# Performance work log

Hardware: AMD Instinct MI355X
Metric: run time of the kernel (lower is better)

The kernel has to match this reference:

```python
import jax, jax.numpy as jnp
import numpy as np

B, T, EI, EO = 64, 512, 1024, 1024

def setup_inputs() -> dict:
    key = jax.random.key(0)
    k1, k2, k3, k4 = jax.random.split(key, 4)
    x = jax.random.normal(k1, (B, T, EI), dtype=jnp.float32)
    h0 = jax.random.normal(k2, (B, EO), dtype=jnp.float32)
    # match nn.Linear init scale roughly (uniform +-1/sqrt(fan_in))
    wxh = jax.random.uniform(k3, (EI, EO), dtype=jnp.float32, minval=-1.0, maxval=1.0) / np.sqrt(EI)
    whf = jax.random.uniform(k4, (EO, EO), dtype=jnp.float32, minval=-1.0, maxval=1.0) / np.sqrt(EO)
    return {"x": x, "h0": h0, "wxh": wxh, "whf": whf}

def reference(x, h0, wxh, whf):
    # Minimal GRU (all NOT_MUTATED flags = 1.0):
    #   ft = sigmoid(h_{t-1} @ whf); gt = tanh(x_t @ wxh)
    #   h_t = (1 - ft) * h_{t-1} + ft * gt; out_t = h_t
    def step(h, xt):
        ft = jax.nn.sigmoid(h @ whf)          # [B, EO]
        gt = jnp.tanh(xt @ wxh)               # [B, EO]
        h = (1.0 - ft) * h + ft * gt
        return h, h
    xT = jnp.swapaxes(x, 0, 1)                # [T, B, EI]
    hT, outs = jax.lax.scan(step, h0, xT)     # outs: [T, B, EO]
    outs = jnp.swapaxes(outs, 0, 1)           # [B, T, EO]
    return outs, hT
```

## Files before the change

kernel.cpp:

```cpp
#include <hip/hip_runtime.h>
#include <stdint.h>

#define B_   64
#define T_   512
#define EI_  1024
#define EO_  1024

typedef __attribute__((ext_vector_type(4))) float  f32x4;
typedef __attribute__((ext_vector_type(8))) short  s16x8;
typedef __attribute__((ext_vector_type(4))) unsigned short u16x4;

__device__ __forceinline__ unsigned short f2bf(float f) {
    union { float f; unsigned int u; } v; v.f = f;
    unsigned int r = v.u + 0x7FFFu + ((v.u >> 16) & 1u);
    return (unsigned short)(r >> 16);
}

__global__ void prep_kernel(const float* __restrict__ wxh, const float* __restrict__ whf,
                            const float* __restrict__ h0,
                            unsigned short* __restrict__ wxhT, unsigned short* __restrict__ whfT,
                            unsigned short* __restrict__ hbf1, unsigned int* __restrict__ flags)
{
    __shared__ unsigned short Ts[64][72];
    const int bid = blockIdx.x;
    const float* src = (bid & 1) ? whf : wxh;
    unsigned short* dst = (bid & 1) ? whfT : wxhT;
    const int tile = bid >> 1;
    const int k0 = (tile >> 4) * 64, n0 = (tile & 15) * 64;
    const int tid = threadIdx.x;

    #pragma unroll
    for (int it = 0; it < 4; ++it) {
        int r  = it * 16 + (tid >> 4);
        int cq = tid & 15;
        f32x4 v = *(const f32x4*)(src + (size_t)(k0 + r) * EO_ + n0 + cq * 4);
        #pragma unroll
        for (int i = 0; i < 4; ++i) Ts[cq * 4 + i][r] = f2bf(v[i]);
    }
    __syncthreads();
    #pragma unroll
    for (int it = 0; it < 2; ++it) {
        int n = it * 32 + (tid >> 3);
        int c = tid & 7;
        s16x8 v = *(const s16x8*)(&Ts[n][c * 8]);
        *(s16x8*)(dst + (size_t)(n0 + n) * EI_ + k0 + c * 8) = v;
    }
    if (bid < 256) {
        int j = bid * 256 + tid;
        hbf1[j] = f2bf(h0[j]);
    }
    if (bid == 0 && tid < 64) flags[tid] = 0u;
}

__launch_bounds__(256, 2)
__global__ void gemm_g_kernel(const float* __restrict__ X,
                              const unsigned short* __restrict__ WT,
                              float* __restrict__ out)
{
    __shared__ alignas(16) unsigned short As[128 * 72];
    __shared__ alignas(16) unsigned short Bs[128 * 72];

    const int bid = blockIdx.x;
    const int bn = bid & 7, bm = bid >> 3;
    const int m0 = bm * 128, n0 = bn * 128;
    const int tid  = threadIdx.x;
    const int lane = tid & 63, w = tid >> 6;
    const int wr = w >> 1, wc = w & 1;
    const int l15 = lane & 15, lg = lane >> 4;

    f32x4 acc[4][4] = {};

    for (int kt = 0; kt < EI_ / 64; ++kt) {
        const int k0 = kt * 64;
        #pragma unroll
        for (int p = 0; p < 8; ++p) {
            int row = p * 16 + (tid >> 4);
            int kq  = tid & 15;
            f32x4 v = *(const f32x4*)(X + (size_t)(m0 + row) * EI_ + k0 + kq * 4);
            u16x4 hv;
            hv[0] = f2bf(v[0]); hv[1] = f2bf(v[1]); hv[2] = f2bf(v[2]); hv[3] = f2bf(v[3]);
            *(u16x4*)(&As[row * 72 + kq * 4]) = hv;
        }
        #pragma unroll
        for (int p = 0; p < 4; ++p) {
            int n  = p * 32 + (tid >> 3);
            int kq = tid & 7;
            s16x8 v = *(const s16x8*)(WT + (size_t)(n0 + n) * EI_ + k0 + kq * 8);
            *(s16x8*)(&Bs[n * 72 + kq * 8]) = v;
        }
        __syncthreads();
        #pragma unroll
        for (int kk = 0; kk < 2; ++kk) {
            s16x8 a[4], b[4];
            #pragma unroll
            for (int mt = 0; mt < 4; ++mt)
                a[mt] = *(const s16x8*)(&As[(wr * 64 + mt * 16 + l15) * 72 + kk * 32 + lg * 8]);
            #pragma unroll
            for (int nt = 0; nt < 4; ++nt)
                b[nt] = *(const s16x8*)(&Bs[(wc * 64 + nt * 16 + l15) * 72 + kk * 32 + lg * 8]);
            #pragma unroll
            for (int mt = 0; mt < 4; ++mt)
                #pragma unroll
                for (int nt = 0; nt < 4; ++nt)
                    acc[mt][nt] = __builtin_amdgcn_mfma_f32_16x16x32_bf16(a[mt], b[nt], acc[mt][nt], 0, 0, 0);
        }
        __syncthreads();
    }
    #pragma unroll
    for (int mt = 0; mt < 4; ++mt) {
        #pragma unroll
        for (int nt = 0; nt < 4; ++nt) {
            #pragma unroll
            for (int r = 0; r < 4; ++r) {
                int row = wr * 64 + mt * 16 + lg * 4 + r;
                int col = wc * 64 + nt * 16 + l15;
                float s = acc[mt][nt][r];
                float e = __expf(2.f * s);
                out[(size_t)(m0 + row) * EO_ + n0 + col] = 1.f - 2.f / (e + 1.f);
            }
        }
    }
}

__launch_bounds__(1024, 1)
__global__ void recur_kernel(const float* __restrict__ h0,
                             const unsigned short* __restrict__ whfT,
                             unsigned short* hbf,
                             unsigned int* flags,
                             float* out)
{
    __shared__ alignas(16) unsigned short Ws[64 * 1024];
    __shared__ float Sred[4 * 16 * 68];

    const int bid = blockIdx.x;
    const int cb = bid >> 4;
    const int cc = bid & 15;
    const int tid = threadIdx.x;
    const int lane = tid & 63, w = tid >> 6;
    const int l15 = lane & 15, lg = lane >> 4;
    const int nq = w & 3, kq = w >> 2;

    {
        int c  = tid >> 4;
        int k8 = tid & 15;
        #pragma unroll
        for (int p = 0; p < 8; ++p) {
            int k = (k8 + p * 16) * 8;
            s16x8 v = *(const s16x8*)(whfT + (size_t)(cc * 64 + c) * EO_ + k);
            *(s16x8*)(&Ws[c * 1024 + (k ^ ((c & 7) << 3))]) = v;
        }
    }

    const int row = tid >> 6;
    const int col = tid & 63;
    const int b = cb * 16 + row;
    const int j = cc * 64 + col;
    float h = h0[(size_t)b * EO_ + j];

    const unsigned int* flg = flags + cb * 16;
    const int wc_frag = nq * 16 + l15;
    const int ksw = (wc_frag & 7) << 3;

    __syncthreads();

    for (int t = 0; t < T_; ++t) {
        size_t oidx = ((size_t)b * T_ + t) * EO_ + j;
        float g = out[oidx];

        if (t > 0 && w == 0) {
            unsigned int want = (unsigned int)t;
            int spins = 0;
            for (;;) {
                unsigned int f = (lane < 16)
                    ? __hip_atomic_load(&flg[lane], __ATOMIC_RELAXED, __HIP_MEMORY_SCOPE_AGENT)
                    : want;
                if (__ballot(f >= want) == ~0ULL) break;
                if (++spins > (1 << 20)) break;
            }
        }
        __syncthreads();

        const unsigned short* arow = hbf + (size_t)((t & 1) ^ 1) * (B_ * EO_)
                                   + (size_t)(cb * 16 + l15) * EO_;
        unsigned long long a0[8], a1[8];
        #pragma unroll
        for (int kk = 0; kk < 8; ++kk) {
            int k = kq * 256 + kk * 32 + lg * 8;
            a0[kk] = __hip_atomic_load((const unsigned long long*)(arow + k),
                                       __ATOMIC_RELAXED, __HIP_MEMORY_SCOPE_AGENT);
            a1[kk] = __hip_atomic_load((const unsigned long long*)(arow + k + 4),
                                       __ATOMIC_RELAXED, __HIP_MEMORY_SCOPE_AGENT);
        }
        f32x4 acc = {0.f, 0.f, 0.f, 0.f};
        #pragma unroll
        for (int kk = 0; kk < 8; ++kk) {
            int k = kq * 256 + kk * 32 + lg * 8;
            s16x8 bb = *(const s16x8*)(&Ws[wc_frag * 1024 + (k ^ ksw)]);
            union { unsigned long long u[2]; s16x8 v; } av;
            av.u[0] = a0[kk]; av.u[1] = a1[kk];
            acc = __builtin_amdgcn_mfma_f32_16x16x32_bf16(av.v, bb, acc, 0, 0, 0);
        }
        #pragma unroll
        for (int r = 0; r < 4; ++r)
            Sred[kq * (16 * 68) + (lg * 4 + r) * 68 + nq * 16 + l15] = acc[r];
        __syncthreads();

        float s = Sred[row * 68 + col]        + Sred[1088 + row * 68 + col]
                + Sred[2176 + row * 68 + col] + Sred[3264 + row * 68 + col];
        float fg = 1.f / (1.f + __expf(-s));
        h = (1.f - fg) * h + fg * g;
        out[oidx] = h;

        unsigned short mybf = f2bf(h);
        unsigned int other = (unsigned int)__shfl_xor((int)(unsigned int)mybf, 1);
        if (!(lane & 1)) {
            unsigned int packed = (unsigned int)mybf | (other << 16);
            __hip_atomic_store((unsigned int*)(hbf + (size_t)(t & 1) * (B_ * EO_)
                                               + (size_t)b * EO_ + j),
                               packed, __ATOMIC_RELAXED, __HIP_MEMORY_SCOPE_AGENT);
        }
        __syncthreads();
        if (tid == 0)
            __hip_atomic_store(&flags[cb * 16 + cc], (unsigned int)(t + 1),
                               __ATOMIC_RELAXED, __HIP_MEMORY_SCOPE_AGENT);
    }
    out[(size_t)B_ * T_ * EO_ + (size_t)b * EO_ + j] = h;
}

extern "C" void kernel_launch(void* const* d_in, const int* in_sizes, int n_in,
                              void* d_out, int out_size, void* d_ws, size_t ws_size,
                              hipStream_t stream)
{
    const float* x   = (const float*)d_in[0];
    const float* h0  = (const float*)d_in[1];
    const float* wxh = (const float*)d_in[2];
    const float* whf = (const float*)d_in[3];
    float* out = (float*)d_out;

    char* ws = (char*)d_ws;
    unsigned short* whfT  = (unsigned short*)(ws);
    unsigned short* wxhT  = (unsigned short*)(ws + (size_t)2 * 1024 * 1024);
    unsigned short* hbf   = (unsigned short*)(ws + (size_t)4 * 1024 * 1024);
    unsigned int*   flags = (unsigned int*)  (ws + (size_t)4 * 1024 * 1024 + 512 * 1024);

    prep_kernel<<<512, 256, 0, stream>>>(wxh, whf, h0, wxhT, whfT, hbf + B_ * EO_, flags);
    gemm_g_kernel<<<2048, 256, 0, stream>>>(x, wxhT, out);
    recur_kernel<<<64, 1024, 0, stream>>>(h0, whfT, hbf, flags, out);
}
```

Measured before the change: 4.495 ms.

## Hold recurrent weights in registers and sync per-wave instead of per-block

The recurrent kernel now runs 256-thread blocks in which each wave keeps its 16-column slice of the recurrent weight matrix in registers (32 fragments) and computes the full K=1024 reduction itself. This removes the LDS weight tile, the cross-wave LDS reduction and all __syncthreads in the time loop. Each wave publishes its own progress flag, and consumers spin on 64 per-wave flags. The cost is heavy register pressure (Wf plus a 64-entry A buffer), which risks spills, along with more flag polling traffic and four times more serial MFMAs per wave on the critical path.

New measurement: 5.628 ms. 25.2% more time.

```diff
diff --git a/kernel.cpp b/kernel.cpp
--- a/kernel.cpp
+++ b/kernel.cpp
@@ -49,7 +49,7 @@
         int j = bid * 256 + tid;
         hbf1[j] = f2bf(h0[j]);
     }
-    if (bid == 0 && tid < 64) flags[tid] = 0u;
+    if (bid == 0) flags[tid] = 0u;
 }
 
 __launch_bounds__(256, 2)
@@ -122,109 +122,98 @@
     }
 }
 
-__launch_bounds__(1024, 1)
+__launch_bounds__(256, 1)
 __global__ void recur_kernel(const float* __restrict__ h0,
                              const unsigned short* __restrict__ whfT,
                              unsigned short* hbf,
                              unsigned int* flags,
                              float* out)
 {
-    __shared__ alignas(16) unsigned short Ws[64 * 1024];
-    __shared__ float Sred[4 * 16 * 68];
-
     const int bid = blockIdx.x;
-    const int cb = bid >> 4;
-    const int cc = bid & 15;
+    const int g = bid >> 4;
+    const int q = bid & 15;
     const int tid = threadIdx.x;
     const int lane = tid & 63, w = tid >> 6;
     const int l15 = lane & 15, lg = lane >> 4;
-    const int nq = w & 3, kq = w >> 2;
-
-    {
-        int c  = tid >> 4;
-        int k8 = tid & 15;
-        #pragma unroll
-        for (int p = 0; p < 8; ++p) {
-            int k = (k8 + p * 16) * 8;
-            s16x8 v = *(const s16x8*)(whfT + (size_t)(cc * 64 + c) * EO_ + k);
-            *(s16x8*)(&Ws[c * 1024 + (k ^ ((c & 7) << 3))]) = v;
-        }
-    }
-
-    const int row = tid >> 6;
-    const int col = tid & 63;
-    const int b = cb * 16 + row;
-    const int j = cc * 64 + col;
-    float h = h0[(size_t)b * EO_ + j];
-
-    const unsigned int* flg = flags + cb * 16;
-    const int wc_frag = nq * 16 + l15;
-    const int ksw = (wc_frag & 7) << 3;
-
-    __syncthreads();
+    const int wid = q * 4 + w;
+    const int col = wid * 16 + l15;
+    const int rowbase = g * 16 + lg * 4;
+
+    s16x8 Wf[32];
+    #pragma unroll
+    for (int kk = 0; kk < 32; ++kk)
+        Wf[kk] = *(const s16x8*)(whfT + (size_t)col * EO_ + kk * 32 + lg * 8);
+
+    float h[4];
+    #pragma unroll
+    for (int r = 0; r < 4; ++r)
+        h[r] = h0[(size_t)(rowbase + r) * EO_ + col];
+
+    unsigned int* const flg = flags + g * 64;
 
     for (int t = 0; t < T_; ++t) {
-        size_t oidx = ((size_t)b * T_ + t) * EO_ + j;
-        float g = out[oidx];
-
-        if (t > 0 && w == 0) {
-            unsigned int want = (unsigned int)t;
+        float gv[4];
+        #pragma unroll
+        for (int r = 0; r < 4; ++r)
+            gv[r] = out[((size_t)(rowbase + r) * T_ + t) * EO_ + col];
+
+        if (t > 0) {
+            const unsigned int want = (unsigned int)t;
             int spins = 0;
             for (;;) {
-                unsigned int f = (lane < 16)
-                    ? __hip_atomic_load(&flg[lane], __ATOMIC_RELAXED, __HIP_MEMORY_SCOPE_AGENT)
-                    : want;
+                unsigned int f = __hip_atomic_load(&flg[lane], __ATOMIC_RELAXED,
+                                                   __HIP_MEMORY_SCOPE_AGENT);
                 if (__ballot(f >= want) == ~0ULL) break;
                 if (++spins > (1 << 20)) break;
             }
         }
-        __syncthreads();
+        asm volatile("" ::: "memory");
 
         const unsigned short* arow = hbf + (size_t)((t & 1) ^ 1) * (B_ * EO_)
-                                   + (size_t)(cb * 16 + l15) * EO_;
-        unsigned long long a0[8], a1[8];
-        #pragma unroll
-        for (int kk = 0; kk < 8; ++kk) {
-            int k = kq * 256 + kk * 32 + lg * 8;
-            a0[kk] = __hip_atomic_load((const unsigned long long*)(arow + k),
-                                       __ATOMIC_RELAXED, __HIP_MEMORY_SCOPE_AGENT);
-            a1[kk] = __hip_atomic_load((const unsigned long long*)(arow + k + 4),
-                                       __ATOMIC_RELAXED, __HIP_MEMORY_SCOPE_AGENT);
-        }
-        f32x4 acc = {0.f, 0.f, 0.f, 0.f};
-        #pragma unroll
-        for (int kk = 0; kk < 8; ++kk) {
-            int k = kq * 256 + kk * 32 + lg * 8;
-            s16x8 bb = *(const s16x8*)(&Ws[wc_frag * 1024 + (k ^ ksw)]);
+                                   + (size_t)(g * 16 + l15) * EO_ + lg * 8;
+        unsigned long long abuf[64];
+        #pragma unroll
+        for (int kk = 0; kk < 32; ++kk) {
+            abuf[2 * kk]     = __hip_atomic_load((const unsigned long long*)(arow + kk * 32),
+                                                 __ATOMIC_RELAXED, __HIP_MEMORY_SCOPE_AGENT);
+            abuf[2 * kk + 1] = __hip_atomic_load((const unsigned long long*)(arow + kk * 32 + 4),
+                                                 __ATOMIC_RELAXED, __HIP_MEMORY_SCOPE_AGENT);
+        }
+        f32x4 acc[4] = {};
+        #pragma unroll
+        for (int kk = 0; kk < 32; ++kk) {
             union { unsigned long long u[2]; s16x8 v; } av;
-            av.u[0] = a0[kk]; av.u[1] = a1[kk];
-            acc = __builtin_amdgcn_mfma_f32_16x16x32_bf16(av.v, bb, acc, 0, 0, 0);
-        }
-        #pragma unroll
-        for (int r = 0; r < 4; ++r)
-            Sred[kq * (16 * 68) + (lg * 4 + r) * 68 + nq * 16 + l15] = acc[r];
-        __syncthreads();
-
-        float s = Sred[row * 68 + col]        + Sred[1088 + row * 68 + col]
-                + Sred[2176 + row * 68 + col] + Sred[3264 + row * 68 + col];
-        float fg = 1.f / (1.f + __expf(-s));
-        h = (1.f - fg) * h + fg * g;
-        out[oidx] = h;
-
-        unsigned short mybf = f2bf(h);
-        unsigned int other = (unsigned int)__shfl_xor((int)(unsigned int)mybf, 1);
-        if (!(lane & 1)) {
-            unsigned int packed = (unsigned int)mybf | (other << 16);
-            __hip_atomic_store((unsigned int*)(hbf + (size_t)(t & 1) * (B_ * EO_)
-                                               + (size_t)b * EO_ + j),
-                               packed, __ATOMIC_RELAXED, __HIP_MEMORY_SCOPE_AGENT);
-        }
-        __syncthreads();
-        if (tid == 0)
-            __hip_atomic_store(&flags[cb * 16 + cc], (unsigned int)(t + 1),
+            av.u[0] = abuf[2 * kk]; av.u[1] = abuf[2 * kk + 1];
+            acc[kk & 3] = __builtin_amdgcn_mfma_f32_16x16x32_bf16(av.v, Wf[kk], acc[kk & 3], 0, 0, 0);
+        }
+
+        unsigned short hb[4];
+        #pragma unroll
+        for (int r = 0; r < 4; ++r) {
+            float s = acc[0][r] + acc[1][r] + acc[2][r] + acc[3][r];
+            float fg = 1.f / (1.f + __expf(-s));
+            h[r] = (1.f - fg) * h[r] + fg * gv[r];
+            out[((size_t)(rowbase + r) * T_ + t) * EO_ + col] = h[r];
+            hb[r] = f2bf(h[r]);
+        }
+        unsigned short* hw = hbf + (size_t)(t & 1) * (B_ * EO_);
+        #pragma unroll
+        for (int r = 0; r < 4; ++r) {
+            unsigned int other = (unsigned int)__shfl_xor((int)(unsigned int)hb[r], 1);
+            if (!(lane & 1)) {
+                unsigned int packed = (unsigned int)hb[r] | (other << 16);
+                __hip_atomic_store((unsigned int*)(hw + (size_t)(rowbase + r) * EO_ + col),
+                                   packed, __ATOMIC_RELAXED, __HIP_MEMORY_SCOPE_AGENT);
+            }
+        }
+        asm volatile("s_waitcnt vmcnt(0)" ::: "memory");
+        if (lane == 0)
+            __hip_atomic_store(&flg[wid], (unsigned int)(t + 1),
                                __ATOMIC_RELAXED, __HIP_MEMORY_SCOPE_AGENT);
     }
-    out[(size_t)B_ * T_ * EO_ + (size_t)b * EO_ + j] = h;
+    #pragma unroll
+    for (int r = 0; r < 4; ++r)
+        out[(size_t)B_ * T_ * EO_ + (size_t)(rowbase + r) * EO_ + col] = h[r];
 }
 
 extern "C" void kernel_launch(void* const* d_in, const int* in_sizes, int n_in,
@@ -245,5 +234,5 @@
 
     prep_kernel<<<512, 256, 0, stream>>>(wxh, whf, h0, wxhT, whfT, hbf + B_ * EO_, flags);
     gemm_g_kernel<<<2048, 256, 0, stream>>>(x, wxhT, out);
-    recur_kernel<<<64, 1024, 0, stream>>>(h0, whfT, hbf, flags, out);
-}
+    recur_kernel<<<64, 256, 0, stream>>>(h0, whfT, hbf, flags, out);
+}
```
